# Performance work log

Hardware: AMD Instinct MI355X
Metric: run time of the kernel (lower is better)

The kernel has to match this reference:

```python
import jax, jax.numpy as jnp
import numpy as np

N_AGENTS = 16384      # number of samples / agents
N_EDGES = 524288      # total relative neighbors (avg degree 32)
FEAT = 4              # relative-neighbor state dim (px, py, vx, vy)
R_AGENT = 0.15        # param.r_agent
BARRIER_MARGIN = 1.2  # hardcoded 1.2 * r_agent in the source


def _glorot(key, shape):
    fan_in = shape[0]
    return jax.random.normal(key, shape, dtype=jnp.float32) / jnp.sqrt(jnp.float32(fan_in))


def setup_inputs() -> dict:
    key = jax.random.key(0)
    ks = jax.random.split(key, 10)
    # Relative positions with |p| in ~[0.7, 3.5] so d - 1.2*r_agent > 0 (physical barrier regime).
    mag = jax.random.uniform(ks[0], (N_EDGES, 2), minval=0.5, maxval=2.5)
    sign = jnp.sign(jax.random.normal(ks[1], (N_EDGES, 2)))
    pos = mag * sign
    vel = 0.1 * jax.random.normal(ks[2], (N_EDGES, 2))
    edge_feats = jnp.concatenate([pos, vel], axis=1)  # [E, 4]
    segment_ids = jnp.sort(jax.random.randint(ks[3], (N_EDGES,), 0, N_AGENTS))
    return {
        "edge_feats": edge_feats,
        "segment_ids": segment_ids,
        "Wp1": _glorot(ks[4], (FEAT, 256)), "bp1": jnp.zeros((256,), jnp.float32),
        "Wp2": _glorot(ks[5], (256, 256)), "bp2": jnp.zeros((256,), jnp.float32),
        "Wp3": _glorot(ks[6], (256, 64)),  "bp3": jnp.zeros((64,), jnp.float32),
        "Wr1": _glorot(ks[7], (64, 256)),  "br1": jnp.zeros((256,), jnp.float32),
        "Wr2": _glorot(ks[8], (256, 256)), "br2": jnp.zeros((256,), jnp.float32),
        "Wr3": _glorot(ks[9], (256, 2)),   "br3": jnp.zeros((2,), jnp.float32),
    }


def reference(edge_feats, segment_ids, Wp1, bp1, Wp2, bp2, Wp3, bp3,
              Wr1, br1, Wr2, br2, Wr3, br3):
    # DeepSet: phi per relative neighbor, sum over each agent's set, rho per agent.
    h = jax.nn.relu(edge_feats @ Wp1 + bp1)          # [E, 256]
    h = jax.nn.relu(h @ Wp2 + bp2)                   # [E, 256]
    h = h @ Wp3 + bp3                                # [E, 64]
    agg = jax.ops.segment_sum(h, segment_ids, num_segments=N_AGENTS)  # [N, 64]
    r = jax.nn.relu(agg @ Wr1 + br1)                 # [N, 256]
    r = jax.nn.relu(r @ Wr2 + br2)                   # [N, 256]
    a_wbarrier = r @ Wr3 + br3                       # [N, 2]

    # Barrier: per edge, -(p/|p|) / (|p| - 1.2*r_agent), scatter-added per agent.
    p = edge_feats[:, :2]                            # [E, 2]
    d = jnp.linalg.norm(p, axis=1, keepdims=True)    # [E, 1]
    contrib = -(p / d) / (d - BARRIER_MARGIN * R_AGENT)  # [E, 2]
    barrier = jax.ops.segment_sum(contrib, segment_ids, num_segments=N_AGENTS)  # [N, 2]

    return a_wbarrier + barrier
```

## Files before the change

kernel.cpp:

```cpp
#include <hip/hip_runtime.h>
#include <hip/hip_bf16.h>

typedef __hip_bfloat16 bf16;
typedef __attribute__((ext_vector_type(8))) short short8;
typedef __attribute__((ext_vector_type(4))) float floatx4;

#define NE 524288
#define NA 16384
#define E  128
#define AG 16
#define S1 260
#define SH3 68

__device__ __forceinline__ float ld(const void* p, long i, int f32) {
    return f32 ? ((const float*)p)[i] : __bfloat162float(((const bf16*)p)[i]);
}
__device__ __forceinline__ short f2bs(float f) {
    bf16 h = __float2bfloat16(f);
    return *(short*)&h;
}
__device__ __forceinline__ float bs2f(short s) {
    union { unsigned u; float f; } c;
    c.u = ((unsigned)(unsigned short)s) << 16;
    return c.f;
}
__device__ __forceinline__ unsigned pk(float a, float b) {
    unsigned r;
    asm("v_cvt_pk_bf16_f32 %0, %1, %2" : "=v"(r) : "v"(a), "v"(b));
    return r;
}

__global__ void prep_weights_kernel(
    const void* __restrict__ Wp1, const void* __restrict__ bp1,
    const void* __restrict__ Wp2, const void* __restrict__ bp2,
    const void* __restrict__ Wp3, const void* __restrict__ bp3,
    const void* __restrict__ Wr1, const void* __restrict__ br1,
    const void* __restrict__ Wr2, const void* __restrict__ br2,
    const void* __restrict__ Wr3, const void* __restrict__ br3,
    short* __restrict__ Wp1P, short* __restrict__ Wp2P, short* __restrict__ Wp3P,
    short* __restrict__ Wr1P,  short* __restrict__ Wr2P,
    float* __restrict__ bp1f, float* __restrict__ bp2f, float* __restrict__ bp3f,
    float* __restrict__ br1f, float* __restrict__ br2f,
    float* __restrict__ Wr3f, float* __restrict__ br3f,
    float* __restrict__ agg,
    int* __restrict__ flag)
{
    const int tid = blockIdx.x * blockDim.x + threadIdx.x;
    const int stride = gridDim.x * blockDim.x;

    {
        const float4 z = { 0.f, 0.f, 0.f, 0.f };
        float4* dst = (float4*)agg;
        for (int i = tid; i < (NA * 66) / 4; i += stride) dst[i] = z;
    }

    __shared__ int sflag;
    if (threadIdx.x < 64) {
        const unsigned short* w = (const unsigned short*)Wp2;
        int bad = 0;
        for (int i = threadIdx.x; i < 1024; i += 64) {
            const int e = (w[i] >> 7) & 0xFF;
            if (e >= 131) bad = 1;
        }
        const unsigned long long m = __ballot(bad);
        if (threadIdx.x == 0) {
            sflag = (m != 0ull) ? 1 : 0;
            if (blockIdx.x == 0) *flag = sflag;
        }
    }
    __syncthreads();
    const int f32 = sflag;

    for (int i = tid; i < 190018; i += stride) {
        if (i < 65536) {
            const int j = i & 7, lane = (i >> 3) & 63;
            const int nt = (i >> 9) & 1, ks = (i >> 10) & 7, w = (i >> 13) & 7;
            const int n = w * 32 + nt * 16 + (lane & 15);
            const int k = ks * 32 + (lane >> 4) * 8 + j;
            Wp2P[i] = f2bs(ld(Wp2, (long)k * 256 + n, f32));
        } else if (i < 98304) {
            const int ii = i - 65536;
            const int j = ii & 7, lane = (ii >> 3) & 63;
            const int ks = (ii >> 9) & 7, w = (ii >> 12) & 7;
            const int n = (w & 3) * 16 + (lane & 15);
            const int k = ks * 32 + (lane >> 4) * 8 + j;
            Wp3P[ii] = f2bs(ld(Wp3, (long)k * 64 + n, f32));
        } else if (i < 106496) {
            const int ii = i - 98304;
            const int j = ii & 7, lane = (ii >> 3) & 63;
            const int nt = (ii >> 9) & 1, w = (ii >> 10) & 7;
            const int n = w * 32 + nt * 16 + (lane & 15);
            const int k = (lane >> 4) * 8 + j;
            Wp1P[ii] = (k < 4) ? f2bs(ld(Wp1, (long)k * 256 + n, f32)) : (short)0;
        } else if (i < 122880) {
            const int ii = i - 106496;
            const int j = ii & 7, lane = (ii >> 3) & 63;
            const int nt = (ii >> 9) & 3, ks = (ii >> 11) & 1, w = (ii >> 12) & 3;
            const int n = w * 64 + nt * 16 + (lane & 15);
            const int k = ks * 32 + (lane >> 4) * 8 + j;
            Wr1P[ii] = f2bs(ld(Wr1, (long)k * 256 + n, f32));
        } else if (i < 188416) {
            const int ii = i - 122880;
            const int j = ii & 7, lane = (ii >> 3) & 63;
            const int nt = (ii >> 9) & 3, ks = (ii >> 11) & 7, w = (ii >> 14) & 3;
            const int n = w * 64 + nt * 16 + (lane & 15);
            const int k = ks * 32 + (lane >> 4) * 8 + j;
            Wr2P[ii] = f2bs(ld(Wr2, (long)k * 256 + n, f32));
        } else if (i < 188672) { bp1f[i - 188416] = ld(bp1, i - 188416, f32); }
        else if (i < 188928) { bp2f[i - 188672] = ld(bp2, i - 188672, f32); }
        else if (i < 188992) { bp3f[i - 188928] = ld(bp3, i - 188928, f32); }
        else if (i < 189248) { br1f[i - 188992] = ld(br1, i - 188992, f32); }
        else if (i < 189504) { br2f[i - 189248] = ld(br2, i - 189248, f32); }
        else if (i < 190016) { Wr3f[i - 189504] = ld(Wr3, i - 189504, f32); }
        else                 { br3f[i - 190016] = ld(br3, i - 190016, f32); }
    }
}

__global__ __launch_bounds__(512, 4) void edge_mlp_kernel(
    const void* __restrict__ ef, const int* __restrict__ ids,
    const short* __restrict__ Wp1P, const float* __restrict__ bp1f,
    const short* __restrict__ Wp2P, const float* __restrict__ bp2f,
    const short* __restrict__ Wp3P, const float* __restrict__ bp3f,
    float* __restrict__ agg, float* __restrict__ bar,
    const int* __restrict__ flag)
{
    __shared__ __align__(16) short hs[E * S1];
    __shared__ float cb[E][2];
    __shared__ int   sid[E];

    const int t = threadIdx.x;
    const int bid = blockIdx.x;
    const int wg = (bid & 7) * ((NE / E) >> 3) + (bid >> 3);
    const long e0 = (long)wg * E;
    const int f32 = *flag;
    const int wave = t >> 6, lane = t & 63, quad = lane >> 4, ln = lane & 15;
    const int nw = wave * 32;
    const int me = (wave >> 2) * 64;
    const int fb = (wave & 3) * 16;

    short8 wcur[2], wnxt[2];
    #pragma unroll
    for (int nt = 0; nt < 2; ++nt)
        wcur[nt] = *(const short8*)&Wp2P[(((wave * 8 + 0) * 2 + nt) * 64 + lane) * 8];
    float4 b1v[2], b2v[2];
    #pragma unroll
    for (int nt = 0; nt < 2; ++nt) {
        b1v[nt] = *(const float4*)&bp1f[nw + nt * 16 + quad * 4];
        b2v[nt] = *(const float4*)&bp2f[nw + nt * 16 + quad * 4];
    }
    short8 w3;
    float4 b3v;

    if (t < E) {
        sid[t] = ids[e0 + t];
        const float px = ld(ef, (e0 + t) * 4 + 0, f32);
        const float py = ld(ef, (e0 + t) * 4 + 1, f32);
        const float d = sqrtf(px * px + py * py);
        const float inv = 1.0f / (d * (d - 0.18f));
        cb[t][0] = -px * inv;
        cb[t][1] = -py * inv;
    }

    {
        short8 b[8];
        #pragma unroll
        for (int mt = 0; mt < 8; ++mt) {
            short8 v = {};
            if (quad == 0) {
                const long e = e0 + mt * 16 + ln;
                if (f32) {
                    const float4 x = ((const float4*)ef)[e];
                    v[0] = f2bs(x.x); v[1] = f2bs(x.y); v[2] = f2bs(x.z); v[3] = f2bs(x.w);
                } else {
                    const int2 x = ((const int2*)ef)[e];
                    v[0] = (short)(x.x & 0xffff); v[1] = (short)((unsigned)x.x >> 16);
                    v[2] = (short)(x.y & 0xffff); v[3] = (short)((unsigned)x.y >> 16);
                }
            }
            b[mt] = v;
        }
        floatx4 acc[8][2];
        #pragma unroll
        for (int nt = 0; nt < 2; ++nt) {
            const floatx4 bi = { b1v[nt].x, b1v[nt].y, b1v[nt].z, b1v[nt].w };
            #pragma unroll
            for (int mt = 0; mt < 8; ++mt) acc[mt][nt] = bi;
        }
        #pragma unroll
        for (int nt = 0; nt < 2; ++nt) {
            const short8 a = *(const short8*)&Wp1P[((wave * 2 + nt) * 64 + lane) * 8];
            #pragma unroll
            for (int mt = 0; mt < 8; ++mt)
                acc[mt][nt] = __builtin_amdgcn_mfma_f32_16x16x32_bf16(a, b[mt], acc[mt][nt], 0, 0, 0);
        }
        #pragma unroll
        for (int mt = 0; mt < 8; ++mt)
            #pragma unroll
            for (int nt = 0; nt < 2; ++nt) {
                const floatx4 v = acc[mt][nt];
                uint2 w;
                w.x = pk(fmaxf(v[0], 0.f), fmaxf(v[1], 0.f));
                w.y = pk(fmaxf(v[2], 0.f), fmaxf(v[3], 0.f));
                *(uint2*)&hs[(mt * 16 + ln) * S1 + nw + nt * 16 + quad * 4] = w;
            }
    }
    __syncthreads();

    {
        floatx4 acc[8][2];
        #pragma unroll
        for (int nt = 0; nt < 2; ++nt) {
            const floatx4 bi = { b2v[nt].x, b2v[nt].y, b2v[nt].z, b2v[nt].w };
            #pragma unroll
            for (int mt = 0; mt < 8; ++mt) acc[mt][nt] = bi;
        }
        #pragma unroll
        for (int ks = 0; ks < 8; ++ks) {
            if (ks < 7) {
                #pragma unroll
                for (int nt = 0; nt < 2; ++nt)
                    wnxt[nt] = *(const short8*)&Wp2P[(((wave * 8 + ks + 1) * 2 + nt) * 64 + lane) * 8];
            }
            #pragma unroll
            for (int mh = 0; mh < 2; ++mh) {
                short8 b[4];
                #pragma unroll
                for (int m4 = 0; m4 < 4; ++m4)
                    b[m4] = *(const short8*)&hs[((mh * 4 + m4) * 16 + ln) * S1 + ks * 32 + quad * 8];
                __builtin_amdgcn_s_setprio(1);
                #pragma unroll
                for (int m4 = 0; m4 < 4; ++m4)
                    #pragma unroll
                    for (int nt = 0; nt < 2; ++nt)
                        acc[mh * 4 + m4][nt] = __builtin_amdgcn_mfma_f32_16x16x32_bf16(wcur[nt], b[m4], acc[mh * 4 + m4][nt], 0, 0, 0);
                __builtin_amdgcn_s_setprio(0);
            }
            #pragma unroll
            for (int nt = 0; nt < 2; ++nt) wcur[nt] = wnxt[nt];
        }
        w3  = *(const short8*)&Wp3P[((wave * 8 + 0) * 64 + lane) * 8];
        b3v = *(const float4*)&bp3f[fb + quad * 4];
        __syncthreads();
        #pragma unroll
        for (int mt = 0; mt < 8; ++mt)
            #pragma unroll
            for (int nt = 0; nt < 2; ++nt) {
                const floatx4 v = acc[mt][nt];
                uint2 w;
                w.x = pk(fmaxf(v[0], 0.f), fmaxf(v[1], 0.f));
                w.y = pk(fmaxf(v[2], 0.f), fmaxf(v[3], 0.f));
                *(uint2*)&hs[(mt * 16 + ln) * S1 + nw + nt * 16 + quad * 4] = w;
            }
    }
    __syncthreads();

    floatx4 acc3[4];
    {
        const floatx4 bi = { b3v.x, b3v.y, b3v.z, b3v.w };
        #pragma unroll
        for (int mt = 0; mt < 4; ++mt) acc3[mt] = bi;
        #pragma unroll
        for (int ks = 0; ks < 8; ++ks) {
            short8 wn = w3;
            if (ks < 7)
                wn = *(const short8*)&Wp3P[((wave * 8 + ks + 1) * 64 + lane) * 8];
            short8 b[4];
            #pragma unroll
            for (int mt = 0; mt < 4; ++mt)
                b[mt] = *(const short8*)&hs[(me + mt * 16 + ln) * S1 + ks * 32 + quad * 8];
            __builtin_amdgcn_s_setprio(1);
            #pragma unroll
            for (int mt = 0; mt < 4; ++mt)
                acc3[mt] = __builtin_amdgcn_mfma_f32_16x16x32_bf16(w3, b[mt], acc3[mt], 0, 0, 0);
            __builtin_amdgcn_s_setprio(0);
            w3 = wn;
        }
    }
    __syncthreads();
    float* h3f = (float*)hs;
    #pragma unroll
    for (int mt = 0; mt < 4; ++mt) {
        float4 v = { acc3[mt][0], acc3[mt][1], acc3[mt][2], acc3[mt][3] };
        *(float4*)&h3f[(me + mt * 16 + ln) * SH3 + fb + quad * 4] = v;
    }
    __syncthreads();

    {
        const int w0 = wave * 16;
        const int f = lane;
        int cur = sid[w0];
        float local = h3f[w0 * SH3 + f];
        #pragma unroll
        for (int e = 1; e < 16; ++e) {
            const int id = sid[w0 + e];
            const float v = h3f[(w0 + e) * SH3 + f];
            if (id == cur) local += v;
            else { atomicAdd(&agg[(long)cur * 64 + f], local); cur = id; local = v; }
        }
        atomicAdd(&agg[(long)cur * 64 + f], local);

        if (lane < 2) {
            int c2 = sid[w0];
            float l2 = cb[w0][lane];
            #pragma unroll
            for (int e = 1; e < 16; ++e) {
                const int id = sid[w0 + e];
                const float v = cb[w0 + e][lane];
                if (id == c2) l2 += v;
                else { atomicAdd(&bar[c2 * 2 + lane], l2); c2 = id; l2 = v; }
            }
            atomicAdd(&bar[c2 * 2 + lane], l2);
        }
    }
}

__global__ __launch_bounds__(256, 4) void agent_mlp_kernel(
    const float* __restrict__ agg, const float* __restrict__ bar,
    const short* __restrict__ Wr1P, const float* __restrict__ br1f,
    const short* __restrict__ Wr2P, const float* __restrict__ br2f,
    const float* __restrict__ Wr3f, const float* __restrict__ br3f,
    void* __restrict__ out, const int* __restrict__ flag)
{
    __shared__ __align__(16) short ha[AG * 68];
    __shared__ __align__(16) short hs[AG * S1];
    __shared__ float part[16][AG][2];

    const int t = threadIdx.x;
    const int a0 = blockIdx.x * AG;
    const int f32 = *flag;
    const int wave = t >> 6, lane = t & 63, quad = lane >> 4, ln = lane & 15;
    const int nb = wave * 64;

    float4 r1b[4], r2b[4];
    #pragma unroll
    for (int nt = 0; nt < 4; ++nt) {
        r1b[nt] = *(const float4*)&br1f[nb + nt * 16 + quad * 4];
        r2b[nt] = *(const float4*)&br2f[nb + nt * 16 + quad * 4];
    }
    short8 a1[4], wcur[4], wnxt[4];
    #pragma unroll
    for (int nt = 0; nt < 4; ++nt) {
        a1[nt]   = *(const short8*)&Wr1P[(((wave * 2 + 0) * 4 + nt) * 64 + lane) * 8];
        wcur[nt] = *(const short8*)&Wr2P[(((wave * 8 + 0) * 4 + nt) * 64 + lane) * 8];
    }
    float barv = 0.f;
    if (t < 2 * AG) barv = bar[(long)a0 * 2 + t];

    {
        const float4 x = ((const float4*)agg)[(long)blockIdx.x * 256 + t];
        uint2 w;
        w.x = pk(x.x, x.y);
        w.y = pk(x.z, x.w);
        *(uint2*)&ha[(t >> 4) * 68 + (t & 15) * 4] = w;
    }
    __syncthreads();

    {
        floatx4 acc[4];
        #pragma unroll
        for (int nt = 0; nt < 4; ++nt)
            acc[nt] = (floatx4){ r1b[nt].x, r1b[nt].y, r1b[nt].z, r1b[nt].w };
        #pragma unroll
        for (int ks = 0; ks < 2; ++ks) {
            const short8 b = *(const short8*)&ha[ln * 68 + ks * 32 + quad * 8];
            short8 a[4];
            #pragma unroll
            for (int nt = 0; nt < 4; ++nt)
                a[nt] = (ks == 0) ? a1[nt]
                      : *(const short8*)&Wr1P[(((wave * 2 + ks) * 4 + nt) * 64 + lane) * 8];
            __builtin_amdgcn_s_setprio(1);
            #pragma unroll
            for (int nt = 0; nt < 4; ++nt)
                acc[nt] = __builtin_amdgcn_mfma_f32_16x16x32_bf16(a[nt], b, acc[nt], 0, 0, 0);
            __builtin_amdgcn_s_setprio(0);
        }
        #pragma unroll
        for (int nt = 0; nt < 4; ++nt) {
            const floatx4 v = acc[nt];
            uint2 w;
            w.x = pk(fmaxf(v[0], 0.f), fmaxf(v[1], 0.f));
            w.y = pk(fmaxf(v[2], 0.f), fmaxf(v[3], 0.f));
            *(uint2*)&hs[ln * S1 + nb + nt * 16 + quad * 4] = w;
        }
    }
    __syncthreads();

    {
        floatx4 acc[4];
        #pragma unroll
        for (int nt = 0; nt < 4; ++nt)
            acc[nt] = (floatx4){ r2b[nt].x, r2b[nt].y, r2b[nt].z, r2b[nt].w };
        #pragma unroll
        for (int ks = 0; ks < 8; ++ks) {
            if (ks < 7) {
                #pragma unroll
                for (int nt = 0; nt < 4; ++nt)
                    wnxt[nt] = *(const short8*)&Wr2P[(((wave * 8 + ks + 1) * 4 + nt) * 64 + lane) * 8];
            }
            const short8 b = *(const short8*)&hs[ln * S1 + ks * 32 + quad * 8];
            __builtin_amdgcn_s_setprio(1);
            #pragma unroll
            for (int nt = 0; nt < 4; ++nt)
                acc[nt] = __builtin_amdgcn_mfma_f32_16x16x32_bf16(wcur[nt], b, acc[nt], 0, 0, 0);
            __builtin_amdgcn_s_setprio(0);
            #pragma unroll
            for (int nt = 0; nt < 4; ++nt) wcur[nt] = wnxt[nt];
        }
        __syncthreads();
        #pragma unroll
        for (int nt = 0; nt < 4; ++nt) {
            const floatx4 v = acc[nt];
            uint2 w;
            w.x = pk(fmaxf(v[0], 0.f), fmaxf(v[1], 0.f));
            w.y = pk(fmaxf(v[2], 0.f), fmaxf(v[3], 0.f));
            *(uint2*)&hs[ln * S1 + nb + nt * 16 + quad * 4] = w;
        }
    }
    __syncthreads();

    {
        const int m = t & 15;
        const int p = t >> 4;
        float v0 = 0.f, v1 = 0.f;
        #pragma unroll
        for (int kk = 0; kk < 2; ++kk) {
            const int k0 = p * 16 + kk * 8;
            const short8 h = *(const short8*)&hs[m * S1 + k0];
            #pragma unroll
            for (int j = 0; j < 8; ++j) {
                const float hv = bs2f(h[j]);
                v0 = fmaf(hv, Wr3f[(k0 + j) * 2 + 0], v0);
                v1 = fmaf(hv, Wr3f[(k0 + j) * 2 + 1], v1);
            }
        }
        part[p][m][0] = v0;
        part[p][m][1] = v1;
    }
    __syncthreads();
    if (t < 2 * AG) {
        const int m = t >> 1, o = t & 1;
        float s = br3f[o] + barv;
        #pragma unroll
        for (int p = 0; p < 16; ++p) s += part[p][m][o];
        if (f32) ((float*)out)[a0 * 2 + t] = s;
        else     ((bf16*)out)[a0 * 2 + t] = __float2bfloat16(s);
    }
}

extern "C" void kernel_launch(void* const* d_in, const int* in_sizes, int n_in,
                              void* d_out, int out_size, void* d_ws, size_t ws_size,
                              hipStream_t stream)
{
    (void)in_sizes; (void)n_in; (void)out_size;

    const void* ef  = d_in[0];
    const int*  ids = (const int*)d_in[1];

    char* p = (char*)d_ws;
    int*   flag  = (int*)p;        p += 256;
    float* agg   = (float*)p;      p += (size_t)NA * 64 * 4;
    float* bar   = (float*)p;      p += (size_t)NA * 2 * 4;
    short* Wp1P  = (short*)p;      p += 8192 * 2;
    short* Wp2P  = (short*)p;      p += 65536 * 2;
    short* Wp3P  = (short*)p;      p += 32768 * 2;
    short* Wr1P  = (short*)p;      p += 16384 * 2;
    short* Wr2P  = (short*)p;      p += 65536 * 2;
    float* bp1f  = (float*)p;      p += 256 * 4;
    float* bp2f  = (float*)p;      p += 256 * 4;
    float* bp3f  = (float*)p;      p += 64 * 4;
    float* br1f  = (float*)p;      p += 256 * 4;
    float* br2f  = (float*)p;      p += 256 * 4;
    float* Wr3f  = (float*)p;      p += 512 * 4;
    float* br3f  = (float*)p;      p += 256;
    const size_t required = (size_t)(p - (char*)d_ws);
    if (ws_size < required) return;

    prep_weights_kernel<<<512, 256, 0, stream>>>(
        d_in[2], d_in[3], d_in[4], d_in[5], d_in[6], d_in[7],
        d_in[8], d_in[9], d_in[10], d_in[11], d_in[12], d_in[13],
        Wp1P, Wp2P, Wp3P, Wr1P, Wr2P,
        bp1f, bp2f, bp3f, br1f, br2f, Wr3f, br3f, agg, flag);
    edge_mlp_kernel<<<NE / E, 512, 0, stream>>>(
        ef, ids, Wp1P, bp1f, Wp2P, bp2f, Wp3P, bp3f, agg, bar, flag);
    agent_mlp_kernel<<<NA / AG, 256, 0, stream>>>(
        agg, bar, Wr1P, br1f, Wr2P, br2f, Wr3f, br3f, d_out, flag);
}
```

Before: 190.2 us.

## Retile edge MLP layers 2 and 3 into square per-wave MFMA blocks

```diff
diff --git a/kernel.cpp b/kernel.cpp
--- a/kernel.cpp
+++ b/kernel.cpp
@@ -71,48 +71,48 @@
     __syncthreads();
     const int f32 = sflag;
 
-    for (int i = tid; i < 190018; i += stride) {
+    for (int i = tid; i < 173634; i += stride) {
         if (i < 65536) {
             const int j = i & 7, lane = (i >> 3) & 63;
-            const int nt = (i >> 9) & 1, ks = (i >> 10) & 7, w = (i >> 13) & 7;
-            const int n = w * 32 + nt * 16 + (lane & 15);
+            const int ks = (i >> 9) & 7, g = (i >> 12) & 15;
+            const int n = g * 16 + (lane & 15);
             const int k = ks * 32 + (lane >> 4) * 8 + j;
             Wp2P[i] = f2bs(ld(Wp2, (long)k * 256 + n, f32));
-        } else if (i < 98304) {
+        } else if (i < 81920) {
             const int ii = i - 65536;
             const int j = ii & 7, lane = (ii >> 3) & 63;
-            const int ks = (ii >> 9) & 7, w = (ii >> 12) & 7;
-            const int n = (w & 3) * 16 + (lane & 15);
+            const int ks = (ii >> 9) & 7, g = (ii >> 12) & 3;
+            const int n = g * 16 + (lane & 15);
             const int k = ks * 32 + (lane >> 4) * 8 + j;
             Wp3P[ii] = f2bs(ld(Wp3, (long)k * 64 + n, f32));
-        } else if (i < 106496) {
-            const int ii = i - 98304;
+        } else if (i < 90112) {
+            const int ii = i - 81920;
             const int j = ii & 7, lane = (ii >> 3) & 63;
             const int nt = (ii >> 9) & 1, w = (ii >> 10) & 7;
             const int n = w * 32 + nt * 16 + (lane & 15);
             const int k = (lane >> 4) * 8 + j;
             Wp1P[ii] = (k < 4) ? f2bs(ld(Wp1, (long)k * 256 + n, f32)) : (short)0;
-        } else if (i < 122880) {
-            const int ii = i - 106496;
+        } else if (i < 106496) {
+            const int ii = i - 90112;
             const int j = ii & 7, lane = (ii >> 3) & 63;
             const int nt = (ii >> 9) & 3, ks = (ii >> 11) & 1, w = (ii >> 12) & 3;
             const int n = w * 64 + nt * 16 + (lane & 15);
             const int k = ks * 32 + (lane >> 4) * 8 + j;
             Wr1P[ii] = f2bs(ld(Wr1, (long)k * 256 + n, f32));
-        } else if (i < 188416) {
-            const int ii = i - 122880;
+        } else if (i < 172032) {
+            const int ii = i - 106496;
             const int j = ii & 7, lane = (ii >> 3) & 63;
             const int nt = (ii >> 9) & 3, ks = (ii >> 11) & 7, w = (ii >> 14) & 3;
             const int n = w * 64 + nt * 16 + (lane & 15);
             const int k = ks * 32 + (lane >> 4) * 8 + j;
             Wr2P[ii] = f2bs(ld(Wr2, (long)k * 256 + n, f32));
-        } else if (i < 188672) { bp1f[i - 188416] = ld(bp1, i - 188416, f32); }
-        else if (i < 188928) { bp2f[i - 188672] = ld(bp2, i - 188672, f32); }
-        else if (i < 188992) { bp3f[i - 188928] = ld(bp3, i - 188928, f32); }
-        else if (i < 189248) { br1f[i - 188992] = ld(br1, i - 188992, f32); }
-        else if (i < 189504) { br2f[i - 189248] = ld(br2, i - 189248, f32); }
-        else if (i < 190016) { Wr3f[i - 189504] = ld(Wr3, i - 189504, f32); }
-        else                 { br3f[i - 190016] = ld(br3, i - 190016, f32); }
+        } else if (i < 172288) { bp1f[i - 172032] = ld(bp1, i - 172032, f32); }
+        else if (i < 172544) { bp2f[i - 172288] = ld(bp2, i - 172288, f32); }
+        else if (i < 172608) { bp3f[i - 172544] = ld(bp3, i - 172544, f32); }
+        else if (i < 172864) { br1f[i - 172608] = ld(br1, i - 172608, f32); }
+        else if (i < 173120) { br2f[i - 172864] = ld(br2, i - 172864, f32); }
+        else if (i < 173632) { Wr3f[i - 173120] = ld(Wr3, i - 173120, f32); }
+        else                 { br3f[i - 173632] = ld(br3, i - 173632, f32); }
     }
 }
 
@@ -134,22 +134,23 @@
     const long e0 = (long)wg * E;
     const int f32 = *flag;
     const int wave = t >> 6, lane = t & 63, quad = lane >> 4, ln = lane & 15;
-    const int nw = wave * 32;
-    const int me = (wave >> 2) * 64;
-    const int fb = (wave & 3) * 16;
-
-    short8 wcur[2], wnxt[2];
+    const int nw  = wave * 32;
+    const int me2 = (wave >> 2) * 64;
+    const int nf2 = (wave & 3) * 64;
+    const int me3 = (wave >> 1) * 32;
+    const int fb3 = (wave & 1) * 32;
+
+    short8 wcur[4], wnxt[4];
+    #pragma unroll
+    for (int nt = 0; nt < 4; ++nt)
+        wcur[nt] = *(const short8*)&Wp2P[((((wave & 3) * 4 + nt) * 8 + 0) * 64 + lane) * 8];
+    float4 b1v[2];
     #pragma unroll
     for (int nt = 0; nt < 2; ++nt)
-        wcur[nt] = *(const short8*)&Wp2P[(((wave * 8 + 0) * 2 + nt) * 64 + lane) * 8];
-    float4 b1v[2], b2v[2];
-    #pragma unroll
-    for (int nt = 0; nt < 2; ++nt) {
         b1v[nt] = *(const float4*)&bp1f[nw + nt * 16 + quad * 4];
-        b2v[nt] = *(const float4*)&bp2f[nw + nt * 16 + quad * 4];
-    }
-    short8 w3;
-    float4 b3v;
+    float4 b2v[4];
+    short8 w3[2];
+    float4 b3v[2];
 
     if (t < E) {
         sid[t] = ids[e0 + t];
@@ -194,6 +195,9 @@
                 acc[mt][nt] = __builtin_amdgcn_mfma_f32_16x16x32_bf16(a, b[mt], acc[mt][nt], 0, 0, 0);
         }
         #pragma unroll
+        for (int nt = 0; nt < 4; ++nt)
+            b2v[nt] = *(const float4*)&bp2f[nf2 + nt * 16 + quad * 4];
+        #pragma unroll
         for (int mt = 0; mt < 8; ++mt)
             #pragma unroll
             for (int nt = 0; nt < 2; ++nt) {
@@ -207,82 +211,95 @@
     __syncthreads();
 
     {
-        floatx4 acc[8][2];
-        #pragma unroll
-        for (int nt = 0; nt < 2; ++nt) {
+        floatx4 acc[4][4];
+        #pragma unroll
+        for (int nt = 0; nt < 4; ++nt) {
             const floatx4 bi = { b2v[nt].x, b2v[nt].y, b2v[nt].z, b2v[nt].w };
             #pragma unroll
-            for (int mt = 0; mt < 8; ++mt) acc[mt][nt] = bi;
+            for (int mt = 0; mt < 4; ++mt) acc[mt][nt] = bi;
         }
         #pragma unroll
         for (int ks = 0; ks < 8; ++ks) {
             if (ks < 7) {
                 #pragma unroll
-                for (int nt = 0; nt < 2; ++nt)
-                    wnxt[nt] = *(const short8*)&Wp2P[(((wave * 8 + ks + 1) * 2 + nt) * 64 + lane) * 8];
-            }
-            #pragma unroll
-            for (int mh = 0; mh < 2; ++mh) {
-                short8 b[4];
+                for (int nt = 0; nt < 4; ++nt)
+                    wnxt[nt] = *(const short8*)&Wp2P[((((wave & 3) * 4 + nt) * 8 + ks + 1) * 64 + lane) * 8];
+            }
+            short8 b[4];
+            #pragma unroll
+            for (int mt = 0; mt < 4; ++mt)
+                b[mt] = *(const short8*)&hs[(me2 + mt * 16 + ln) * S1 + ks * 32 + quad * 8];
+            __builtin_amdgcn_s_setprio(1);
+            #pragma unroll
+            for (int mt = 0; mt < 4; ++mt)
                 #pragma unroll
-                for (int m4 = 0; m4 < 4; ++m4)
-                    b[m4] = *(const short8*)&hs[((mh * 4 + m4) * 16 + ln) * S1 + ks * 32 + quad * 8];
-                __builtin_amdgcn_s_setprio(1);
-                #pragma unroll
-                for (int m4 = 0; m4 < 4; ++m4)
-                    #pragma unroll
-                    for (int nt = 0; nt < 2; ++nt)
-                        acc[mh * 4 + m4][nt] = __builtin_amdgcn_mfma_f32_16x16x32_bf16(wcur[nt], b[m4], acc[mh * 4 + m4][nt], 0, 0, 0);
-                __builtin_amdgcn_s_setprio(0);
-            }
-            #pragma unroll
-            for (int nt = 0; nt < 2; ++nt) wcur[nt] = wnxt[nt];
-        }
-        w3  = *(const short8*)&Wp3P[((wave * 8 + 0) * 64 + lane) * 8];
-        b3v = *(const float4*)&bp3f[fb + quad * 4];
+                for (int nt = 0; nt < 4; ++nt)
+                    acc[mt][nt] = __builtin_amdgcn_mfma_f32_16x16x32_bf16(wcur[nt], b[mt], acc[mt][nt], 0, 0, 0);
+            __builtin_amdgcn_s_setprio(0);
+            #pragma unroll
+            for (int nt = 0; nt < 4; ++nt) wcur[nt] = wnxt[nt];
+        }
+        #pragma unroll
+        for (int nt = 0; nt < 2; ++nt) {
+            w3[nt]  = *(const short8*)&Wp3P[((((wave & 1) * 2 + nt) * 8 + 0) * 64 + lane) * 8];
+            b3v[nt] = *(const float4*)&bp3f[fb3 + nt * 16 + quad * 4];
+        }
         __syncthreads();
         #pragma unroll
-        for (int mt = 0; mt < 8; ++mt)
-            #pragma unroll
-            for (int nt = 0; nt < 2; ++nt) {
+        for (int mt = 0; mt < 4; ++mt)
+            #pragma unroll
+            for (int nt = 0; nt < 4; ++nt) {
                 const floatx4 v = acc[mt][nt];
                 uint2 w;
                 w.x = pk(fmaxf(v[0], 0.f), fmaxf(v[1], 0.f));
                 w.y = pk(fmaxf(v[2], 0.f), fmaxf(v[3], 0.f));
-                *(uint2*)&hs[(mt * 16 + ln) * S1 + nw + nt * 16 + quad * 4] = w;
-            }
-    }
-    __syncthreads();
-
-    floatx4 acc3[4];
-    {
-        const floatx4 bi = { b3v.x, b3v.y, b3v.z, b3v.w };
-        #pragma unroll
-        for (int mt = 0; mt < 4; ++mt) acc3[mt] = bi;
+                *(uint2*)&hs[(me2 + mt * 16 + ln) * S1 + nf2 + nt * 16 + quad * 4] = w;
+            }
+    }
+    __syncthreads();
+
+    floatx4 acc3[2][2];
+    {
+        #pragma unroll
+        for (int nt = 0; nt < 2; ++nt) {
+            const floatx4 bi = { b3v[nt].x, b3v[nt].y, b3v[nt].z, b3v[nt].w };
+            #pragma unroll
+            for (int mt = 0; mt < 2; ++mt) acc3[mt][nt] = bi;
+        }
         #pragma unroll
         for (int ks = 0; ks < 8; ++ks) {
-            short8 wn = w3;
-            if (ks < 7)
-                wn = *(const short8*)&Wp3P[((wave * 8 + ks + 1) * 64 + lane) * 8];
-            short8 b[4];
-            #pragma unroll
-            for (int mt = 0; mt < 4; ++mt)
-                b[mt] = *(const short8*)&hs[(me + mt * 16 + ln) * S1 + ks * 32 + quad * 8];
+            short8 wn_[2];
+            if (ks < 7) {
+                #pragma unroll
+                for (int nt = 0; nt < 2; ++nt)
+                    wn_[nt] = *(const short8*)&Wp3P[((((wave & 1) * 2 + nt) * 8 + ks + 1) * 64 + lane) * 8];
+            }
+            short8 b[2];
+            #pragma unroll
+            for (int mt = 0; mt < 2; ++mt)
+                b[mt] = *(const short8*)&hs[(me3 + mt * 16 + ln) * S1 + ks * 32 + quad * 8];
             __builtin_amdgcn_s_setprio(1);
             #pragma unroll
-            for (int mt = 0; mt < 4; ++mt)
-                acc3[mt] = __builtin_amdgcn_mfma_f32_16x16x32_bf16(w3, b[mt], acc3[mt], 0, 0, 0);
+            for (int mt = 0; mt < 2; ++mt)
+                #pragma unroll
+                for (int nt = 0; nt < 2; ++nt)
+                    acc3[mt][nt] = __builtin_amdgcn_mfma_f32_16x16x32_bf16(w3[nt], b[mt], acc3[mt][nt], 0, 0, 0);
             __builtin_amdgcn_s_setprio(0);
-            w3 = wn;
+            if (ks < 7) {
+                #pragma unroll
+                for (int nt = 0; nt < 2; ++nt) w3[nt] = wn_[nt];
+            }
         }
     }
     __syncthreads();
     float* h3f = (float*)hs;
     #pragma unroll
-    for (int mt = 0; mt < 4; ++mt) {
-        float4 v = { acc3[mt][0], acc3[mt][1], acc3[mt][2], acc3[mt][3] };
-        *(float4*)&h3f[(me + mt * 16 + ln) * SH3 + fb + quad * 4] = v;
-    }
+    for (int mt = 0; mt < 2; ++mt)
+        #pragma unroll
+        for (int nt = 0; nt < 2; ++nt) {
+            float4 v = { acc3[mt][nt][0], acc3[mt][nt][1], acc3[mt][nt][2], acc3[mt][nt][3] };
+            *(float4*)&h3f[(me3 + mt * 16 + ln) * SH3 + fb3 + nt * 16 + quad * 4] = v;
+        }
     __syncthreads();
 
     {
@@ -462,7 +479,7 @@
     float* bar   = (float*)p;      p += (size_t)NA * 2 * 4;
     short* Wp1P  = (short*)p;      p += 8192 * 2;
     short* Wp2P  = (short*)p;      p += 65536 * 2;
-    short* Wp3P  = (short*)p;      p += 32768 * 2;
+    short* Wp3P  = (short*)p;      p += 16384 * 2;
     short* Wr1P  = (short*)p;      p += 16384 * 2;
     short* Wr2P  = (short*)p;      p += 65536 * 2;
     float* bp1f  = (float*)p;      p += 256 * 4;
```

Result: slower. 204.7 us (+7.7%).

## Give each wave its own 16 edge rows in layer 3 to drop block barriers

Applied to the files above, without the earlier changes.

```diff
diff --git a/kernel.cpp b/kernel.cpp
--- a/kernel.cpp
+++ b/kernel.cpp
@@ -10,7 +10,6 @@
 #define E  128
 #define AG 16
 #define S1 260
-#define SH3 68
 
 __device__ __forceinline__ float ld(const void* p, long i, int f32) {
     return f32 ? ((const float*)p)[i] : __bfloat162float(((const bf16*)p)[i]);
@@ -71,48 +70,48 @@
     __syncthreads();
     const int f32 = sflag;
 
-    for (int i = tid; i < 190018; i += stride) {
+    for (int i = tid; i < 173634; i += stride) {
         if (i < 65536) {
             const int j = i & 7, lane = (i >> 3) & 63;
             const int nt = (i >> 9) & 1, ks = (i >> 10) & 7, w = (i >> 13) & 7;
             const int n = w * 32 + nt * 16 + (lane & 15);
             const int k = ks * 32 + (lane >> 4) * 8 + j;
             Wp2P[i] = f2bs(ld(Wp2, (long)k * 256 + n, f32));
-        } else if (i < 98304) {
+        } else if (i < 81920) {
             const int ii = i - 65536;
             const int j = ii & 7, lane = (ii >> 3) & 63;
-            const int ks = (ii >> 9) & 7, w = (ii >> 12) & 7;
-            const int n = (w & 3) * 16 + (lane & 15);
+            const int ks = (ii >> 9) & 7, g = (ii >> 12) & 3;
+            const int n = g * 16 + (lane & 15);
             const int k = ks * 32 + (lane >> 4) * 8 + j;
             Wp3P[ii] = f2bs(ld(Wp3, (long)k * 64 + n, f32));
-        } else if (i < 106496) {
-            const int ii = i - 98304;
+        } else if (i < 90112) {
+            const int ii = i - 81920;
             const int j = ii & 7, lane = (ii >> 3) & 63;
             const int nt = (ii >> 9) & 1, w = (ii >> 10) & 7;
             const int n = w * 32 + nt * 16 + (lane & 15);
             const int k = (lane >> 4) * 8 + j;
             Wp1P[ii] = (k < 4) ? f2bs(ld(Wp1, (long)k * 256 + n, f32)) : (short)0;
-        } else if (i < 122880) {
-            const int ii = i - 106496;
+        } else if (i < 106496) {
+            const int ii = i - 90112;
             const int j = ii & 7, lane = (ii >> 3) & 63;
             const int nt = (ii >> 9) & 3, ks = (ii >> 11) & 1, w = (ii >> 12) & 3;
             const int n = w * 64 + nt * 16 + (lane & 15);
             const int k = ks * 32 + (lane >> 4) * 8 + j;
             Wr1P[ii] = f2bs(ld(Wr1, (long)k * 256 + n, f32));
-        } else if (i < 188416) {
-            const int ii = i - 122880;
+        } else if (i < 172032) {
+            const int ii = i - 106496;
             const int j = ii & 7, lane = (ii >> 3) & 63;
             const int nt = (ii >> 9) & 3, ks = (ii >> 11) & 7, w = (ii >> 14) & 3;
             const int n = w * 64 + nt * 16 + (lane & 15);
             const int k = ks * 32 + (lane >> 4) * 8 + j;
             Wr2P[ii] = f2bs(ld(Wr2, (long)k * 256 + n, f32));
-        } else if (i < 188672) { bp1f[i - 188416] = ld(bp1, i - 188416, f32); }
-        else if (i < 188928) { bp2f[i - 188672] = ld(bp2, i - 188672, f32); }
-        else if (i < 188992) { bp3f[i - 188928] = ld(bp3, i - 188928, f32); }
-        else if (i < 189248) { br1f[i - 188992] = ld(br1, i - 188992, f32); }
-        else if (i < 189504) { br2f[i - 189248] = ld(br2, i - 189248, f32); }
-        else if (i < 190016) { Wr3f[i - 189504] = ld(Wr3, i - 189504, f32); }
-        else                 { br3f[i - 190016] = ld(br3, i - 190016, f32); }
+        } else if (i < 172288) { bp1f[i - 172032] = ld(bp1, i - 172032, f32); }
+        else if (i < 172544) { bp2f[i - 172288] = ld(bp2, i - 172288, f32); }
+        else if (i < 172608) { bp3f[i - 172544] = ld(bp3, i - 172544, f32); }
+        else if (i < 172864) { br1f[i - 172608] = ld(br1, i - 172608, f32); }
+        else if (i < 173120) { br2f[i - 172864] = ld(br2, i - 172864, f32); }
+        else if (i < 173632) { Wr3f[i - 173120] = ld(Wr3, i - 173120, f32); }
+        else                 { br3f[i - 173632] = ld(br3, i - 173632, f32); }
     }
 }
 
@@ -135,8 +134,7 @@
     const int f32 = *flag;
     const int wave = t >> 6, lane = t & 63, quad = lane >> 4, ln = lane & 15;
     const int nw = wave * 32;
-    const int me = (wave >> 2) * 64;
-    const int fb = (wave & 3) * 16;
+    const int w0 = wave * 16;
 
     short8 wcur[2], wnxt[2];
     #pragma unroll
@@ -148,8 +146,8 @@
         b1v[nt] = *(const float4*)&bp1f[nw + nt * 16 + quad * 4];
         b2v[nt] = *(const float4*)&bp2f[nw + nt * 16 + quad * 4];
     }
-    short8 w3;
-    float4 b3v;
+    short8 w3[4];
+    float4 b3v[4];
 
     if (t < E) {
         sid[t] = ids[e0 + t];
@@ -238,8 +236,11 @@
             #pragma unroll
             for (int nt = 0; nt < 2; ++nt) wcur[nt] = wnxt[nt];
         }
-        w3  = *(const short8*)&Wp3P[((wave * 8 + 0) * 64 + lane) * 8];
-        b3v = *(const float4*)&bp3f[fb + quad * 4];
+        #pragma unroll
+        for (int nt = 0; nt < 4; ++nt) {
+            w3[nt]  = *(const short8*)&Wp3P[((nt * 8 + 0) * 64 + lane) * 8];
+            b3v[nt] = *(const float4*)&bp3f[nt * 16 + quad * 4];
+        }
         __syncthreads();
         #pragma unroll
         for (int mt = 0; mt < 8; ++mt)
@@ -256,44 +257,46 @@
 
     floatx4 acc3[4];
     {
-        const floatx4 bi = { b3v.x, b3v.y, b3v.z, b3v.w };
-        #pragma unroll
-        for (int mt = 0; mt < 4; ++mt) acc3[mt] = bi;
+        #pragma unroll
+        for (int nt = 0; nt < 4; ++nt)
+            acc3[nt] = (floatx4){ b3v[nt].x, b3v[nt].y, b3v[nt].z, b3v[nt].w };
         #pragma unroll
         for (int ks = 0; ks < 8; ++ks) {
-            short8 wn = w3;
-            if (ks < 7)
-                wn = *(const short8*)&Wp3P[((wave * 8 + ks + 1) * 64 + lane) * 8];
-            short8 b[4];
-            #pragma unroll
-            for (int mt = 0; mt < 4; ++mt)
-                b[mt] = *(const short8*)&hs[(me + mt * 16 + ln) * S1 + ks * 32 + quad * 8];
+            short8 wn_[4];
+            if (ks < 7) {
+                #pragma unroll
+                for (int nt = 0; nt < 4; ++nt)
+                    wn_[nt] = *(const short8*)&Wp3P[((nt * 8 + ks + 1) * 64 + lane) * 8];
+            }
+            const short8 b = *(const short8*)&hs[(w0 + ln) * S1 + ks * 32 + quad * 8];
             __builtin_amdgcn_s_setprio(1);
             #pragma unroll
-            for (int mt = 0; mt < 4; ++mt)
-                acc3[mt] = __builtin_amdgcn_mfma_f32_16x16x32_bf16(w3, b[mt], acc3[mt], 0, 0, 0);
+            for (int nt = 0; nt < 4; ++nt)
+                acc3[nt] = __builtin_amdgcn_mfma_f32_16x16x32_bf16(w3[nt], b, acc3[nt], 0, 0, 0);
             __builtin_amdgcn_s_setprio(0);
-            w3 = wn;
-        }
-    }
-    __syncthreads();
-    float* h3f = (float*)hs;
-    #pragma unroll
-    for (int mt = 0; mt < 4; ++mt) {
-        float4 v = { acc3[mt][0], acc3[mt][1], acc3[mt][2], acc3[mt][3] };
-        *(float4*)&h3f[(me + mt * 16 + ln) * SH3 + fb + quad * 4] = v;
-    }
-    __syncthreads();
-
-    {
-        const int w0 = wave * 16;
+            if (ks < 7) {
+                #pragma unroll
+                for (int nt = 0; nt < 4; ++nt) w3[nt] = wn_[nt];
+            }
+        }
+    }
+    {
+        float* hr = (float*)&hs[(w0 + ln) * S1];
+        #pragma unroll
+        for (int nt = 0; nt < 4; ++nt) {
+            *(float2*)&hr[nt * 16 + quad * 4]     = (float2){ acc3[nt][0], acc3[nt][1] };
+            *(float2*)&hr[nt * 16 + quad * 4 + 2] = (float2){ acc3[nt][2], acc3[nt][3] };
+        }
+    }
+
+    {
         const int f = lane;
         int cur = sid[w0];
-        float local = h3f[w0 * SH3 + f];
+        float local = ((const float*)&hs[w0 * S1])[f];
         #pragma unroll
         for (int e = 1; e < 16; ++e) {
             const int id = sid[w0 + e];
-            const float v = h3f[(w0 + e) * SH3 + f];
+            const float v = ((const float*)&hs[(w0 + e) * S1])[f];
             if (id == cur) local += v;
             else { atomicAdd(&agg[(long)cur * 64 + f], local); cur = id; local = v; }
         }
@@ -462,7 +465,7 @@
     float* bar   = (float*)p;      p += (size_t)NA * 2 * 4;
     short* Wp1P  = (short*)p;      p += 8192 * 2;
     short* Wp2P  = (short*)p;      p += 65536 * 2;
-    short* Wp3P  = (short*)p;      p += 32768 * 2;
+    short* Wp3P  = (short*)p;      p += 16384 * 2;
     short* Wr1P  = (short*)p;      p += 16384 * 2;
     short* Wr2P  = (short*)p;      p += 65536 * 2;
     float* bp1f  = (float*)p;      p += 256 * 4;
```

Result: slower. 204.4 us (+7.5%).

## Process two edge tiles per block with async LDS prefetch of next tile

Applied to the files above, without the earlier changes.

```diff
diff --git a/kernel.cpp b/kernel.cpp
--- a/kernel.cpp
+++ b/kernel.cpp
@@ -4,6 +4,7 @@
 typedef __hip_bfloat16 bf16;
 typedef __attribute__((ext_vector_type(8))) short short8;
 typedef __attribute__((ext_vector_type(4))) float floatx4;
+typedef __attribute__((ext_vector_type(4))) short s16x4;
 
 #define NE 524288
 #define NA 16384
@@ -28,6 +29,16 @@
     unsigned r;
     asm("v_cvt_pk_bf16_f32 %0, %1, %2" : "=v"(r) : "v"(a), "v"(b));
     return r;
+}
+__device__ __forceinline__ void gll16(const void* g, void* l) {
+    __builtin_amdgcn_global_load_lds(
+        (const __attribute__((address_space(1))) unsigned*)g,
+        (__attribute__((address_space(3))) unsigned*)l, 16, 0, 0);
+}
+__device__ __forceinline__ void gll4(const void* g, void* l) {
+    __builtin_amdgcn_global_load_lds(
+        (const __attribute__((address_space(1))) unsigned*)g,
+        (__attribute__((address_space(3))) unsigned*)l, 4, 0, 0);
 }
 
 __global__ void prep_weights_kernel(
@@ -42,8 +53,7 @@
     float* __restrict__ bp1f, float* __restrict__ bp2f, float* __restrict__ bp3f,
     float* __restrict__ br1f, float* __restrict__ br2f,
     float* __restrict__ Wr3f, float* __restrict__ br3f,
-    float* __restrict__ agg,
-    int* __restrict__ flag)
+    float* __restrict__ agg, int* __restrict__ flag)
 {
     const int tid = blockIdx.x * blockDim.x + threadIdx.x;
     const int stride = gridDim.x * blockDim.x;
@@ -127,189 +137,229 @@
     __shared__ __align__(16) short hs[E * S1];
     __shared__ float cb[E][2];
     __shared__ int   sid[E];
+    __shared__ __align__(16) char stg_ef[2048];
+    __shared__ __align__(16) int  stg_id[E];
 
     const int t = threadIdx.x;
     const int bid = blockIdx.x;
-    const int wg = (bid & 7) * ((NE / E) >> 3) + (bid >> 3);
-    const long e0 = (long)wg * E;
+    const int wg = (bid & 7) * ((NE / E / 2) >> 3) + (bid >> 3);
     const int f32 = *flag;
     const int wave = t >> 6, lane = t & 63, quad = lane >> 4, ln = lane & 15;
     const int nw = wave * 32;
     const int me = (wave >> 2) * 64;
     const int fb = (wave & 3) * 16;
 
-    short8 wcur[2], wnxt[2];
-    #pragma unroll
-    for (int nt = 0; nt < 2; ++nt)
-        wcur[nt] = *(const short8*)&Wp2P[(((wave * 8 + 0) * 2 + nt) * 64 + lane) * 8];
-    float4 b1v[2], b2v[2];
-    #pragma unroll
-    for (int nt = 0; nt < 2; ++nt) {
-        b1v[nt] = *(const float4*)&bp1f[nw + nt * 16 + quad * 4];
-        b2v[nt] = *(const float4*)&bp2f[nw + nt * 16 + quad * 4];
-    }
-    short8 w3;
-    float4 b3v;
-
-    if (t < E) {
-        sid[t] = ids[e0 + t];
-        const float px = ld(ef, (e0 + t) * 4 + 0, f32);
-        const float py = ld(ef, (e0 + t) * 4 + 1, f32);
-        const float d = sqrtf(px * px + py * py);
-        const float inv = 1.0f / (d * (d - 0.18f));
-        cb[t][0] = -px * inv;
-        cb[t][1] = -py * inv;
-    }
-
     {
-        short8 b[8];
-        #pragma unroll
-        for (int mt = 0; mt < 8; ++mt) {
-            short8 v = {};
-            if (quad == 0) {
-                const long e = e0 + mt * 16 + ln;
-                if (f32) {
-                    const float4 x = ((const float4*)ef)[e];
-                    v[0] = f2bs(x.x); v[1] = f2bs(x.y); v[2] = f2bs(x.z); v[3] = f2bs(x.w);
-                } else {
-                    const int2 x = ((const int2*)ef)[e];
-                    v[0] = (short)(x.x & 0xffff); v[1] = (short)((unsigned)x.x >> 16);
-                    v[2] = (short)(x.y & 0xffff); v[3] = (short)((unsigned)x.y >> 16);
-                }
-            }
-            b[mt] = v;
-        }
-        floatx4 acc[8][2];
+        const long e0s = (long)wg * 2 * E;
+        if (wave == 0) {
+            if (f32) {
+                gll16((const char*)ef + (e0s + lane) * 16,        stg_ef);
+                gll16((const char*)ef + (e0s + 64 + lane) * 16,   stg_ef + 1024);
+            } else {
+                gll16((const char*)ef + e0s * 8 + (long)lane * 16, stg_ef);
+            }
+        }
+        if (wave == 1) {
+            gll4(ids + e0s + lane,      stg_id);
+            gll4(ids + e0s + 64 + lane, stg_id + 64);
+        }
+    }
+
+    for (int tt = 0; tt < 2; ++tt) {
+        const long e0 = ((long)wg * 2 + tt) * E;
+
+        if (wave < 2) asm volatile("s_waitcnt vmcnt(0)" ::: "memory");
+        __syncthreads();
+
+        if (t < E) {
+            sid[t] = stg_id[t];
+            float px, py;
+            if (f32) { px = ((const float*)stg_ef)[t * 4 + 0]; py = ((const float*)stg_ef)[t * 4 + 1]; }
+            else     { px = bs2f(((const short*)stg_ef)[t * 4 + 0]); py = bs2f(((const short*)stg_ef)[t * 4 + 1]); }
+            const float d = sqrtf(px * px + py * py);
+            const float inv = 1.0f / (d * (d - 0.18f));
+            cb[t][0] = -px * inv;
+            cb[t][1] = -py * inv;
+        }
+
+        short8 wcur[2], wnxt[2];
+        #pragma unroll
+        for (int nt = 0; nt < 2; ++nt)
+            wcur[nt] = *(const short8*)&Wp2P[(((wave * 8 + 0) * 2 + nt) * 64 + lane) * 8];
+        float4 b1v[2], b2v[2];
         #pragma unroll
         for (int nt = 0; nt < 2; ++nt) {
-            const floatx4 bi = { b1v[nt].x, b1v[nt].y, b1v[nt].z, b1v[nt].w };
-            #pragma unroll
-            for (int mt = 0; mt < 8; ++mt) acc[mt][nt] = bi;
-        }
-        #pragma unroll
-        for (int nt = 0; nt < 2; ++nt) {
-            const short8 a = *(const short8*)&Wp1P[((wave * 2 + nt) * 64 + lane) * 8];
+            b1v[nt] = *(const float4*)&bp1f[nw + nt * 16 + quad * 4];
+            b2v[nt] = *(const float4*)&bp2f[nw + nt * 16 + quad * 4];
+        }
+        short8 w3;
+        float4 b3v;
+
+        {
+            short8 b[8];
+            #pragma unroll
+            for (int mt = 0; mt < 8; ++mt) {
+                short8 v = {};
+                if (quad == 0) {
+                    const int e = mt * 16 + ln;
+                    if (f32) {
+                        const float4 x = ((const float4*)stg_ef)[e];
+                        v[0] = f2bs(x.x); v[1] = f2bs(x.y); v[2] = f2bs(x.z); v[3] = f2bs(x.w);
+                    } else {
+                        const s16x4 x4 = ((const s16x4*)stg_ef)[e];
+                        v[0] = x4.x; v[1] = x4.y; v[2] = x4.z; v[3] = x4.w;
+                    }
+                }
+                b[mt] = v;
+            }
+            floatx4 acc[8][2];
+            #pragma unroll
+            for (int nt = 0; nt < 2; ++nt) {
+                const floatx4 bi = { b1v[nt].x, b1v[nt].y, b1v[nt].z, b1v[nt].w };
+                #pragma unroll
+                for (int mt = 0; mt < 8; ++mt) acc[mt][nt] = bi;
+            }
+            #pragma unroll
+            for (int nt = 0; nt < 2; ++nt) {
+                const short8 a = *(const short8*)&Wp1P[((wave * 2 + nt) * 64 + lane) * 8];
+                #pragma unroll
+                for (int mt = 0; mt < 8; ++mt)
+                    acc[mt][nt] = __builtin_amdgcn_mfma_f32_16x16x32_bf16(a, b[mt], acc[mt][nt], 0, 0, 0);
+            }
             #pragma unroll
             for (int mt = 0; mt < 8; ++mt)
-                acc[mt][nt] = __builtin_amdgcn_mfma_f32_16x16x32_bf16(a, b[mt], acc[mt][nt], 0, 0, 0);
-        }
-        #pragma unroll
-        for (int mt = 0; mt < 8; ++mt)
+                #pragma unroll
+                for (int nt = 0; nt < 2; ++nt) {
+                    const floatx4 v = acc[mt][nt];
+                    uint2 w;
+                    w.x = pk(fmaxf(v[0], 0.f), fmaxf(v[1], 0.f));
+                    w.y = pk(fmaxf(v[2], 0.f), fmaxf(v[3], 0.f));
+                    *(uint2*)&hs[(mt * 16 + ln) * S1 + nw + nt * 16 + quad * 4] = w;
+                }
+        }
+        __syncthreads();
+
+        {
+            floatx4 acc[8][2];
             #pragma unroll
             for (int nt = 0; nt < 2; ++nt) {
-                const floatx4 v = acc[mt][nt];
-                uint2 w;
-                w.x = pk(fmaxf(v[0], 0.f), fmaxf(v[1], 0.f));
-                w.y = pk(fmaxf(v[2], 0.f), fmaxf(v[3], 0.f));
-                *(uint2*)&hs[(mt * 16 + ln) * S1 + nw + nt * 16 + quad * 4] = w;
-            }
-    }
-    __syncthreads();
-
-    {
-        floatx4 acc[8][2];
-        #pragma unroll
-        for (int nt = 0; nt < 2; ++nt) {
-            const floatx4 bi = { b2v[nt].x, b2v[nt].y, b2v[nt].z, b2v[nt].w };
-            #pragma unroll
-            for (int mt = 0; mt < 8; ++mt) acc[mt][nt] = bi;
-        }
-        #pragma unroll
-        for (int ks = 0; ks < 8; ++ks) {
-            if (ks < 7) {
-                #pragma unroll
-                for (int nt = 0; nt < 2; ++nt)
-                    wnxt[nt] = *(const short8*)&Wp2P[(((wave * 8 + ks + 1) * 2 + nt) * 64 + lane) * 8];
-            }
-            #pragma unroll
-            for (int mh = 0; mh < 2; ++mh) {
-                short8 b[4];
-                #pragma unroll
-                for (int m4 = 0; m4 < 4; ++m4)
-                    b[m4] = *(const short8*)&hs[((mh * 4 + m4) * 16 + ln) * S1 + ks * 32 + quad * 8];
-                __builtin_amdgcn_s_setprio(1);
-                #pragma unroll
-                for (int m4 = 0; m4 < 4; ++m4)
+                const floatx4 bi = { b2v[nt].x, b2v[nt].y, b2v[nt].z, b2v[nt].w };
+                #pragma unroll
+                for (int mt = 0; mt < 8; ++mt) acc[mt][nt] = bi;
+            }
+            #pragma unroll
+            for (int ks = 0; ks < 8; ++ks) {
+                if (ks < 7) {
                     #pragma unroll
                     for (int nt = 0; nt < 2; ++nt)
-                        acc[mh * 4 + m4][nt] = __builtin_amdgcn_mfma_f32_16x16x32_bf16(wcur[nt], b[m4], acc[mh * 4 + m4][nt], 0, 0, 0);
+                        wnxt[nt] = *(const short8*)&Wp2P[(((wave * 8 + ks + 1) * 2 + nt) * 64 + lane) * 8];
+                }
+                #pragma unroll
+                for (int mh = 0; mh < 2; ++mh) {
+                    short8 b[4];
+                    #pragma unroll
+                    for (int m4 = 0; m4 < 4; ++m4)
+                        b[m4] = *(const short8*)&hs[((mh * 4 + m4) * 16 + ln) * S1 + ks * 32 + quad * 8];
+                    __builtin_amdgcn_s_setprio(1);
+                    #pragma unroll
+                    for (int m4 = 0; m4 < 4; ++m4)
+                        #pragma unroll
+                        for (int nt = 0; nt < 2; ++nt)
+                            acc[mh * 4 + m4][nt] = __builtin_amdgcn_mfma_f32_16x16x32_bf16(wcur[nt], b[m4], acc[mh * 4 + m4][nt], 0, 0, 0);
+                    __builtin_amdgcn_s_setprio(0);
+                }
+                #pragma unroll
+                for (int nt = 0; nt < 2; ++nt) wcur[nt] = wnxt[nt];
+            }
+            w3  = *(const short8*)&Wp3P[((wave * 8 + 0) * 64 + lane) * 8];
+            b3v = *(const float4*)&bp3f[fb + quad * 4];
+            __syncthreads();
+            #pragma unroll
+            for (int mt = 0; mt < 8; ++mt)
+                #pragma unroll
+                for (int nt = 0; nt < 2; ++nt) {
+                    const floatx4 v = acc[mt][nt];
+                    uint2 w;
+                    w.x = pk(fmaxf(v[0], 0.f), fmaxf(v[1], 0.f));
+                    w.y = pk(fmaxf(v[2], 0.f), fmaxf(v[3], 0.f));
+                    *(uint2*)&hs[(mt * 16 + ln) * S1 + nw + nt * 16 + quad * 4] = w;
+                }
+        }
+        __syncthreads();
+
+        if (tt == 0) {
+            const long e1 = e0 + E;
+            if (wave == 0) {
+                if (f32) {
+                    gll16((const char*)ef + (e1 + lane) * 16,      stg_ef);
+                    gll16((const char*)ef + (e1 + 64 + lane) * 16, stg_ef + 1024);
+                } else {
+                    gll16((const char*)ef + e1 * 8 + (long)lane * 16, stg_ef);
+                }
+            }
+            if (wave == 1) {
+                gll4(ids + e1 + lane,      stg_id);
+                gll4(ids + e1 + 64 + lane, stg_id + 64);
+            }
+        }
+
+        floatx4 acc3[4];
+        {
+            const floatx4 bi = { b3v.x, b3v.y, b3v.z, b3v.w };
+            #pragma unroll
+            for (int mt = 0; mt < 4; ++mt) acc3[mt] = bi;
+            #pragma unroll
+            for (int ks = 0; ks < 8; ++ks) {
+                short8 wn = w3;
+                if (ks < 7)
+                    wn = *(const short8*)&Wp3P[((wave * 8 + ks + 1) * 64 + lane) * 8];
+                short8 b[4];
+                #pragma unroll
+                for (int mt = 0; mt < 4; ++mt)
+                    b[mt] = *(const short8*)&hs[(me + mt * 16 + ln) * S1 + ks * 32 + quad * 8];
+                __builtin_amdgcn_s_setprio(1);
+                #pragma unroll
+                for (int mt = 0; mt < 4; ++mt)
+                    acc3[mt] = __builtin_amdgcn_mfma_f32_16x16x32_bf16(w3, b[mt], acc3[mt], 0, 0, 0);
                 __builtin_amdgcn_s_setprio(0);
-            }
-            #pragma unroll
-            for (int nt = 0; nt < 2; ++nt) wcur[nt] = wnxt[nt];
-        }
-        w3  = *(const short8*)&Wp3P[((wave * 8 + 0) * 64 + lane) * 8];
-        b3v = *(const float4*)&bp3f[fb + quad * 4];
+                w3 = wn;
+            }
+        }
         __syncthreads();
-        #pragma unroll
-        for (int mt = 0; mt < 8; ++mt)
-            #pragma unroll
-            for (int nt = 0; nt < 2; ++nt) {
-                const floatx4 v = acc[mt][nt];
-                uint2 w;
-                w.x = pk(fmaxf(v[0], 0.f), fmaxf(v[1], 0.f));
-                w.y = pk(fmaxf(v[2], 0.f), fmaxf(v[3], 0.f));
-                *(uint2*)&hs[(mt * 16 + ln) * S1 + nw + nt * 16 + quad * 4] = w;
-            }
-    }
-    __syncthreads();
-
-    floatx4 acc3[4];
-    {
-        const floatx4 bi = { b3v.x, b3v.y, b3v.z, b3v.w };
-        #pragma unroll
-        for (int mt = 0; mt < 4; ++mt) acc3[mt] = bi;
-        #pragma unroll
-        for (int ks = 0; ks < 8; ++ks) {
-            short8 wn = w3;
-            if (ks < 7)
-                wn = *(const short8*)&Wp3P[((wave * 8 + ks + 1) * 64 + lane) * 8];
-            short8 b[4];
-            #pragma unroll
-            for (int mt = 0; mt < 4; ++mt)
-                b[mt] = *(const short8*)&hs[(me + mt * 16 + ln) * S1 + ks * 32 + quad * 8];
-            __builtin_amdgcn_s_setprio(1);
-            #pragma unroll
-            for (int mt = 0; mt < 4; ++mt)
-                acc3[mt] = __builtin_amdgcn_mfma_f32_16x16x32_bf16(w3, b[mt], acc3[mt], 0, 0, 0);
-            __builtin_amdgcn_s_setprio(0);
-            w3 = wn;
-        }
-    }
-    __syncthreads();
-    float* h3f = (float*)hs;
-    #pragma unroll
-    for (int mt = 0; mt < 4; ++mt) {
-        float4 v = { acc3[mt][0], acc3[mt][1], acc3[mt][2], acc3[mt][3] };
-        *(float4*)&h3f[(me + mt * 16 + ln) * SH3 + fb + quad * 4] = v;
-    }
-    __syncthreads();
-
-    {
-        const int w0 = wave * 16;
-        const int f = lane;
-        int cur = sid[w0];
-        float local = h3f[w0 * SH3 + f];
-        #pragma unroll
-        for (int e = 1; e < 16; ++e) {
-            const int id = sid[w0 + e];
-            const float v = h3f[(w0 + e) * SH3 + f];
-            if (id == cur) local += v;
-            else { atomicAdd(&agg[(long)cur * 64 + f], local); cur = id; local = v; }
-        }
-        atomicAdd(&agg[(long)cur * 64 + f], local);
-
-        if (lane < 2) {
-            int c2 = sid[w0];
-            float l2 = cb[w0][lane];
+        float* h3f = (float*)hs;
+        #pragma unroll
+        for (int mt = 0; mt < 4; ++mt) {
+            float4 v = { acc3[mt][0], acc3[mt][1], acc3[mt][2], acc3[mt][3] };
+            *(float4*)&h3f[(me + mt * 16 + ln) * SH3 + fb + quad * 4] = v;
+        }
+        __syncthreads();
+
+        {
+            const int w0 = wave * 16;
+            const int f = lane;
+            int cur = sid[w0];
+            float local = h3f[w0 * SH3 + f];
             #pragma unroll
             for (int e = 1; e < 16; ++e) {
                 const int id = sid[w0 + e];
-                const float v = cb[w0 + e][lane];
-                if (id == c2) l2 += v;
-                else { atomicAdd(&bar[c2 * 2 + lane], l2); c2 = id; l2 = v; }
-            }
-            atomicAdd(&bar[c2 * 2 + lane], l2);
+                const float v = h3f[(w0 + e) * SH3 + f];
+                if (id == cur) local += v;
+                else { atomicAdd(&agg[(long)cur * 64 + f], local); cur = id; local = v; }
+            }
+            atomicAdd(&agg[(long)cur * 64 + f], local);
+
+            if (lane < 2) {
+                int c2 = sid[w0];
+                float l2 = cb[w0][lane];
+                #pragma unroll
+                for (int e = 1; e < 16; ++e) {
+                    const int id = sid[w0 + e];
+                    const float v = cb[w0 + e][lane];
+                    if (id == c2) l2 += v;
+                    else { atomicAdd(&bar[c2 * 2 + lane], l2); c2 = id; l2 = v; }
+                }
+                atomicAdd(&bar[c2 * 2 + lane], l2);
+            }
         }
     }
 }
@@ -480,7 +530,7 @@
         d_in[8], d_in[9], d_in[10], d_in[11], d_in[12], d_in[13],
         Wp1P, Wp2P, Wp3P, Wr1P, Wr2P,
         bp1f, bp2f, bp3f, br1f, br2f, Wr3f, br3f, agg, flag);
-    edge_mlp_kernel<<<NE / E, 512, 0, stream>>>(
+    edge_mlp_kernel<<<NE / E / 2, 512, 0, stream>>>(
         ef, ids, Wp1P, bp1f, Wp2P, bp2f, Wp3P, bp3f, agg, bar, flag);
     agent_mlp_kernel<<<NA / AG, 256, 0, stream>>>(
         agg, bar, Wr1P, br1f, Wr2P, br2f, Wr3f, br3f, d_out, flag);
```

After: 270.8 us. 1.42x slower.
